# Kernel tuning notes

Hardware: AMD Instinct MI355X
Metric: run time of the kernel (lower is better)

Reference implementation:

```python
import jax, jax.numpy as jnp
import numpy as np

N_NODES = 50000
N_RAND_EDGES = 800000
IN_DIM = 128
HEADS = 4
OUT_FEATS = 32
NEG_SLOPE = 0.2  # DGL GATConv default


def setup_inputs() -> dict:
    key = jax.random.key(0)
    k1, k2, k3, k4, k5, k6 = jax.random.split(key, 6)
    h = jax.random.normal(k1, (N_NODES, IN_DIM), dtype=jnp.float32)
    fc_w = jax.random.normal(k2, (HEADS * OUT_FEATS, IN_DIM), dtype=jnp.float32) * 0.1
    attn_l = jax.random.normal(k3, (HEADS, OUT_FEATS), dtype=jnp.float32) * 0.1
    attn_r = jax.random.normal(k4, (HEADS, OUT_FEATS), dtype=jnp.float32) * 0.1
    src_r = jax.random.randint(k5, (N_RAND_EDGES,), 0, N_NODES, dtype=jnp.int32)
    dst_r = jax.random.randint(k6, (N_RAND_EDGES,), 0, N_NODES, dtype=jnp.int32)
    loops = jnp.arange(N_NODES, dtype=jnp.int32)
    src = jnp.concatenate([src_r, loops])  # self-loops ensure in_degree >= 1
    dst = jnp.concatenate([dst_r, loops])
    return {"h": h, "fc_w": fc_w, "attn_l": attn_l, "attn_r": attn_r,
            "src": src, "dst": dst}


def reference(h, fc_w, attn_l, attn_r, src, dst):
    N = h.shape[0]
    # linear projection, reshape to [N, H, D]
    hf = (h @ fc_w.T).reshape(N, HEADS, OUT_FEATS)
    # per-node attention halves: el = <hf, a_l>, er = <hf, a_r>  -> [N, H]
    el = jnp.einsum('nhd,hd->nh', hf, attn_l)
    er = jnp.einsum('nhd,hd->nh', hf, attn_r)
    # edge scores: u_add_v + leaky_relu  -> [E, H]
    e = jax.nn.leaky_relu(el[src] + er[dst], negative_slope=NEG_SLOPE)
    # segment softmax over incoming edges of each dst node
    m = jax.ops.segment_max(e, dst, num_segments=N)
    ex = jnp.exp(e - m[dst])
    s = jax.ops.segment_sum(ex, dst, num_segments=N)
    a = ex / s[dst]  # [E, H]
    # weighted neighbor aggregation: u_mul_e then segment sum
    msg = hf[src] * a[:, :, None]  # [E, H, D]
    out = jax.ops.segment_sum(msg, dst, num_segments=N)  # [N, H, D]
    return out.reshape(N, HEADS * OUT_FEATS), a[:, :, None]
```

## Files before the change

kernel.cpp:

```cpp
#include <hip/hip_runtime.h>
#include <hip/hip_bf16.h>

#define NEG 0.2f
#define BSTRIDE 8192

typedef float vf4 __attribute__((ext_vector_type(4)));
typedef int   vi4 __attribute__((ext_vector_type(4)));
typedef short bf8 __attribute__((ext_vector_type(8)));
typedef float f32x4 __attribute__((ext_vector_type(4)));

__device__ __forceinline__ float leaky(float x){ return x > 0.f ? x : NEG*x; }
__device__ __forceinline__ float sel4(float4 q, int head){
  float lo = (head & 1) ? q.y : q.x;
  float hi = (head & 1) ? q.w : q.z;
  return (head & 2) ? hi : lo;
}
__device__ __forceinline__ float b2f_lo(unsigned u){ return __uint_as_float(u << 16); }
__device__ __forceinline__ float b2f_hi(unsigned u){ return __uint_as_float(u & 0xffff0000u); }
__device__ __forceinline__ float b2f(unsigned short u){ return __uint_as_float((unsigned)u << 16); }
__device__ __forceinline__ unsigned short f2b(float f){
  __hip_bfloat16 b = __float2bfloat16(f);
  return *(unsigned short*)&b;
}
__device__ __forceinline__ void ntstore_f4(float* p, float a, float b, float c, float d){
  vf4 v; v.x = a; v.y = b; v.z = c; v.w = d;
  __builtin_nontemporal_store(v, (vf4*)p);
}

__global__ __launch_bounds__(256) void k_proj(
    const float* __restrict__ h, const float* __restrict__ fcw,
    const float* __restrict__ attn_l, const float* __restrict__ attn_r,
    unsigned short* __restrict__ hf16, float* __restrict__ el, float* __restrict__ er,
    int* __restrict__ bcur, int N)
{
  __shared__ __align__(16) unsigned short fcs[128*128];
  __shared__ __align__(16) unsigned short hs[4][16*128];

  const int tid = threadIdx.x;
  if (blockIdx.x == 0) bcur[tid] = tid * BSTRIDE;

  for (int i = tid; i < 128*16; i += 256) {
    int f = i >> 4, ch = i & 15;
    const float* p = &fcw[(size_t)f*128 + ch*8];
    float4 w0 = *(const float4*)p;
    float4 w1 = *(const float4*)(p + 4);
    unsigned short* q = &fcs[f*128 + (ch ^ (f & 7))*8];
    q[0]=f2b(w0.x); q[1]=f2b(w0.y); q[2]=f2b(w0.z); q[3]=f2b(w0.w);
    q[4]=f2b(w1.x); q[5]=f2b(w1.y); q[6]=f2b(w1.z); q[7]=f2b(w1.w);
  }
  __syncthreads();

  const int wave = tid >> 6, lane = tid & 63;
  const int r = lane & 15, khi = lane >> 4;

  for (int nt = 0; nt < 2; ++nt) {
    const int nb0 = blockIdx.x*128 + nt*64 + wave*16;
    int gn_a = nb0 + r; if (gn_a >= N) gn_a = N-1;
    const float* hp = &h[(size_t)gn_a*128];

    bf8 afr[4];
    #pragma unroll
    for (int ks = 0; ks < 4; ++ks) {
      const float* p = hp + ks*32 + khi*8;
      float4 w0 = *(const float4*)p;
      float4 w1 = *(const float4*)(p + 4);
      bf8 a;
      a[0]=(short)f2b(w0.x); a[1]=(short)f2b(w0.y); a[2]=(short)f2b(w0.z); a[3]=(short)f2b(w0.w);
      a[4]=(short)f2b(w1.x); a[5]=(short)f2b(w1.y); a[6]=(short)f2b(w1.z); a[7]=(short)f2b(w1.w);
      afr[ks] = a;
    }

    f32x4 acc[8];
    #pragma unroll
    for (int ct = 0; ct < 8; ++ct) { acc[ct][0]=0.f; acc[ct][1]=0.f; acc[ct][2]=0.f; acc[ct][3]=0.f; }

    #pragma unroll
    for (int ct = 0; ct < 8; ++ct) {
      const int f = ct*16 + r;
      #pragma unroll
      for (int ks = 0; ks < 4; ++ks) {
        const int ch = (ks*4 + khi) ^ (f & 7);
        bf8 b = *(const bf8*)&fcs[f*128 + ch*8];
        acc[ct] = __builtin_amdgcn_mfma_f32_16x16x32_bf16(afr[ks], b, acc[ct], 0, 0, 0);
      }
    }

    unsigned short* hw = &hs[wave][0];
    #pragma unroll
    for (int ct = 0; ct < 8; ++ct) {
      const int ftile = ct*16 + r;
      #pragma unroll
      for (int j = 0; j < 4; ++j)
        hw[(khi*4 + j)*128 + ftile] = f2b(acc[ct][j]);
    }

    for (int i = lane; i < 16*16; i += 64) {
      int row = i >> 4, ch = i & 15;
      int gn = nb0 + row;
      if (gn < N)
        *(uint4*)&hf16[(size_t)gn*128 + ch*8] = *(const uint4*)&hw[row*128 + ch*8];
    }

    {
      const int row = lane >> 2, head = lane & 3;
      const int gn = nb0 + row;
      const unsigned short* hr = &hw[row*128 + head*32];
      const float* alp = &attn_l[head*32];
      const float* arp = &attn_r[head*32];
      float e_l = 0.f, e_r = 0.f;
      #pragma unroll
      for (int ff = 0; ff < 32; ++ff) {
        float hv = b2f(hr[ff]);
        e_l += hv * alp[ff];
        e_r += hv * arp[ff];
      }
      if (gn < N) {
        el[(size_t)gn*4 + head] = e_l;
        er[(size_t)gn*4 + head] = e_r;
      }
    }
  }
}

#define TILE 4096
__global__ __launch_bounds__(1024) void k_bin(
    const int* __restrict__ src, const int* __restrict__ dst,
    int* __restrict__ bcur, unsigned int* __restrict__ staging, int E)
{
  __shared__ unsigned int lpack[TILE];
  __shared__ unsigned char lbkt[TILE];
  __shared__ unsigned short sidx[TILE];
  __shared__ int lhist[256], lbase[256], lcur[256], gbase[256];

  const int t = threadIdx.x;
  const int e0 = blockIdx.x * TILE;
  const int cnt = min(TILE, E - e0);

  if (t < 256) lhist[t] = 0;
  __syncthreads();

  for (int i = t; i < cnt; i += 1024) {
    int s = __builtin_nontemporal_load(&src[e0 + i]);
    int d = __builtin_nontemporal_load(&dst[e0 + i]);
    lpack[i] = ((unsigned)(d & 255) << 24) | (unsigned)s;
    int b = d >> 8;
    lbkt[i] = (unsigned char)b;
    atomicAdd(&lhist[b], 1);
  }
  __syncthreads();

  __shared__ int ltmp[256];
  if (t < 256) ltmp[t] = lhist[t];
  __syncthreads();
  for (int off = 1; off < 256; off <<= 1) {
    int x = 0;
    if (t < 256 && t >= off) x = ltmp[t - off];
    __syncthreads();
    if (t < 256) ltmp[t] += x;
    __syncthreads();
  }
  if (t < 256) { lbase[t] = ltmp[t] - lhist[t]; lcur[t] = ltmp[t] - lhist[t]; }
  __syncthreads();

  for (int i = t; i < cnt; i += 1024) {
    int p = atomicAdd(&lcur[lbkt[i]], 1);
    sidx[p] = (unsigned short)i;
  }
  if (t < 256) {
    int c = lhist[t];
    gbase[t] = c ? atomicAdd(&bcur[t], c) : 0;
  }
  __syncthreads();

  for (int p = t; p < cnt; p += 1024) {
    int j = sidx[p];
    int b = lbkt[j];
    staging[gbase[b] + (p - lbase[b])] = lpack[j];
  }
}

__global__ __launch_bounds__(1024) void k_debin(
    const unsigned int* __restrict__ staging, const int* __restrict__ bcur,
    int* __restrict__ esrc, int* __restrict__ offsets, int* __restrict__ degs, int N)
{
  __shared__ int lout[BSTRIDE];
  __shared__ int lhist[256], lexcl[256], lcur[256];

  const int t = threadIdx.x;
  const int b = blockIdx.x;
  const int n0 = b << 8;
  const int nb = min(256, N - n0);
  const int out_start = b * BSTRIDE;
  const int cnt = bcur[b] - out_start;

  if (t < 256) lhist[t] = 0;
  __syncthreads();

  for (int i = t; i < cnt; i += 1024)
    atomicAdd(&lhist[staging[out_start + i] >> 24], 1);
  __syncthreads();

  if (t < 256) lexcl[t] = lhist[t];
  __syncthreads();
  for (int off = 1; off < 256; off <<= 1) {
    int x = 0;
    if (t < 256 && t >= off) x = lexcl[t - off];
    __syncthreads();
    if (t < 256) lexcl[t] += x;
    __syncthreads();
  }
  if (t < 256) {
    int ex = lexcl[t] - lhist[t];
    lexcl[t] = ex;
    lcur[t]  = ex;
  }
  __syncthreads();

  for (int i = t; i < cnt; i += 1024) {
    unsigned int w = staging[out_start + i];
    int p = atomicAdd(&lcur[w >> 24], 1);
    lout[p] = (int)(w & 0x00FFFFFFu);
  }
  __syncthreads();
  for (int i = t; i < cnt; i += 1024)
    esrc[out_start + i] = lout[i];

  if (t < nb) {
    offsets[n0 + t] = out_start + lexcl[t];
    degs[n0 + t]    = lhist[t];
  }
}

__global__ __launch_bounds__(256) void k_aggr(
    const int* __restrict__ esrc, const int* __restrict__ offsets, const int* __restrict__ degs,
    const unsigned short* __restrict__ hf16, const float* __restrict__ el, const float* __restrict__ er,
    float* __restrict__ out, float* __restrict__ mr, int N)
{
  __shared__ float as[4][64][4];
  __shared__ int   es[4][64];
  const int wave = threadIdx.x >> 6, lane = threadIdx.x & 63;
  const int v = blockIdx.x*4 + wave;
  if (v >= N) return;
  const int start = offsets[v];
  const int deg   = degs[v];
  const float4 er4 = *(const float4*)&er[(size_t)v*4];

  const bool act = lane < deg;
  float4 x4 = make_float4(0.f, 0.f, 0.f, 0.f);
  int mys = 0;
  if (act) {
    mys = esrc[start + lane];
    float4 el4 = *(const float4*)&el[(size_t)mys*4];
    x4.x = __expf(leaky(el4.x + er4.x));
    x4.y = __expf(leaky(el4.y + er4.y));
    x4.z = __expf(leaky(el4.z + er4.z));
    x4.w = __expf(leaky(el4.w + er4.w));
  }
  float4 s4 = x4;
  for (int j = lane + 64; j < deg; j += 64) {
    int s = esrc[start + j];
    float4 el4 = *(const float4*)&el[(size_t)s*4];
    s4.x += __expf(leaky(el4.x + er4.x));
    s4.y += __expf(leaky(el4.y + er4.y));
    s4.z += __expf(leaky(el4.z + er4.z));
    s4.w += __expf(leaky(el4.w + er4.w));
  }
  #pragma unroll
  for (int mm = 32; mm; mm >>= 1) {
    s4.x += __shfl_xor(s4.x, mm);
    s4.y += __shfl_xor(s4.y, mm);
    s4.z += __shfl_xor(s4.z, mm);
    s4.w += __shfl_xor(s4.w, mm);
  }
  const float4 r4 = make_float4(1.f/s4.x, 1.f/s4.y, 1.f/s4.z, 1.f/s4.w);

  if (act) {
    float4 a4 = make_float4(x4.x*r4.x, x4.y*r4.y, x4.z*r4.z, x4.w*r4.w);
    *(float4*)&as[wave][lane][0] = a4;
    es[wave][lane] = mys;
  }
  if (lane == 0) *(float4*)&mr[(size_t)v*4] = r4;

  const int g = lane >> 3;
  const int l = lane & 7;
  const int head = l >> 1;
  float acc[16];
  #pragma unroll
  for (int k = 0; k < 16; ++k) acc[k] = 0.f;

  const int degL = deg < 64 ? deg : 64;
  {
    int je = g;
    int jec = je < degL ? je : 0;
    int sj = es[wave][jec];
    float a = je < degL ? as[wave][jec][head] : 0.f;
    const unsigned short* hp = &hf16[(size_t)sj*128 + 16*l];
    uint4 q0 = *(const uint4*)hp;
    uint4 q1 = *(const uint4*)(hp + 8);
    for (int j = 0; j < degL; j += 8) {
      int je2 = j + 8 + g;
      int jec2 = je2 < degL ? je2 : 0;
      int s2 = es[wave][jec2];
      float a2 = je2 < degL ? as[wave][jec2][head] : 0.f;
      const unsigned short* hp2 = &hf16[(size_t)s2*128 + 16*l];
      uint4 p0 = *(const uint4*)hp2;
      uint4 p1 = *(const uint4*)(hp2 + 8);
      acc[0]  += a*b2f_lo(q0.x); acc[1]  += a*b2f_hi(q0.x);
      acc[2]  += a*b2f_lo(q0.y); acc[3]  += a*b2f_hi(q0.y);
      acc[4]  += a*b2f_lo(q0.z); acc[5]  += a*b2f_hi(q0.z);
      acc[6]  += a*b2f_lo(q0.w); acc[7]  += a*b2f_hi(q0.w);
      acc[8]  += a*b2f_lo(q1.x); acc[9]  += a*b2f_hi(q1.x);
      acc[10] += a*b2f_lo(q1.y); acc[11] += a*b2f_hi(q1.y);
      acc[12] += a*b2f_lo(q1.z); acc[13] += a*b2f_hi(q1.z);
      acc[14] += a*b2f_lo(q1.w); acc[15] += a*b2f_hi(q1.w);
      q0 = p0; q1 = p1; a = a2;
    }
  }
  for (int j = 64; j < deg; j += 8) {
    const int je = j + g;
    const bool valid = je < deg;
    int s = esrc[start + (valid ? je : 0)];
    float rh = sel4(r4, head), erh = sel4(er4, head);
    float a = __expf(leaky(el[(size_t)s*4 + head] + erh)) * rh;
    if (!valid) a = 0.f;
    const unsigned short* hp = &hf16[(size_t)s*128 + 16*l];
    uint4 q0 = *(const uint4*)hp;
    uint4 q1 = *(const uint4*)(hp + 8);
    acc[0]  += a*b2f_lo(q0.x); acc[1]  += a*b2f_hi(q0.x);
    acc[2]  += a*b2f_lo(q0.y); acc[3]  += a*b2f_hi(q0.y);
    acc[4]  += a*b2f_lo(q0.z); acc[5]  += a*b2f_hi(q0.z);
    acc[6]  += a*b2f_lo(q0.w); acc[7]  += a*b2f_hi(q0.w);
    acc[8]  += a*b2f_lo(q1.x); acc[9]  += a*b2f_hi(q1.x);
    acc[10] += a*b2f_lo(q1.y); acc[11] += a*b2f_hi(q1.y);
    acc[12] += a*b2f_lo(q1.z); acc[13] += a*b2f_hi(q1.z);
    acc[14] += a*b2f_lo(q1.w); acc[15] += a*b2f_hi(q1.w);
  }

  #pragma unroll
  for (int k = 0; k < 16; ++k) {
    acc[k] += __shfl_xor(acc[k], 8);
    acc[k] += __shfl_xor(acc[k], 16);
    acc[k] += __shfl_xor(acc[k], 32);
  }
  if (g == 0) {
    float* op = &out[(size_t)v*128 + 16*l];
    ntstore_f4(op,      acc[0],  acc[1],  acc[2],  acc[3]);
    ntstore_f4(op + 4,  acc[4],  acc[5],  acc[6],  acc[7]);
    ntstore_f4(op + 8,  acc[8],  acc[9],  acc[10], acc[11]);
    ntstore_f4(op + 12, acc[12], acc[13], acc[14], acc[15]);
  }
}

__global__ void k_attn(const int* __restrict__ src, const int* __restrict__ dst,
                       const float* __restrict__ el, const float* __restrict__ er,
                       const float* __restrict__ mr, float* __restrict__ a_out, int E) {
  int e = blockIdx.x*256 + threadIdx.x;
  if (e >= E) return;
  int s = __builtin_nontemporal_load(&src[e]);
  int d = __builtin_nontemporal_load(&dst[e]);
  float4 el4 = *(const float4*)&el[(size_t)s*4];
  float4 er4 = *(const float4*)&er[(size_t)d*4];
  float4 c4  = *(const float4*)&mr[(size_t)d*4];
  float ax = __expf(leaky(el4.x + er4.x)) * c4.x;
  float ay = __expf(leaky(el4.y + er4.y)) * c4.y;
  float az = __expf(leaky(el4.z + er4.z)) * c4.z;
  float aw = __expf(leaky(el4.w + er4.w)) * c4.w;
  ntstore_f4(&a_out[(size_t)e*4], ax, ay, az, aw);
}

extern "C" void kernel_launch(void* const* d_in, const int* in_sizes, int n_in,
                              void* d_out, int out_size, void* d_ws, size_t ws_size,
                              hipStream_t stream) {
  const float* h      = (const float*)d_in[0];
  const float* fcw    = (const float*)d_in[1];
  const float* attn_l = (const float*)d_in[2];
  const float* attn_r = (const float*)d_in[3];
  const int*   src    = (const int*)d_in[4];
  const int*   dst    = (const int*)d_in[5];
  const int N = in_sizes[0] / 128;
  const int E = in_sizes[4];
  const int B = (N + 255) >> 8;

  float* out   = (float*)d_out;
  float* a_out = out + (size_t)N*128;

  char* w = (char*)d_ws;
  unsigned short* hf16 = (unsigned short*)w; w += (size_t)N*128*sizeof(unsigned short);
  float* el      = (float*)w; w += (size_t)N*4*sizeof(float);
  float* er      = (float*)w; w += (size_t)N*4*sizeof(float);
  float* mr      = (float*)w; w += (size_t)N*4*sizeof(float);
  int*   esrc    = (int*)w;   w += (size_t)256*BSTRIDE*sizeof(int);
  unsigned int* staging = (unsigned int*)w; w += (size_t)256*BSTRIDE*sizeof(unsigned int);
  int*   offsets = (int*)w;   w += (size_t)N*sizeof(int);
  int*   degs    = (int*)w;   w += (size_t)N*sizeof(int);
  int*   bcur    = (int*)w;   w += 256*sizeof(int);

  k_proj<<<(N + 127)/128, 256, 0, stream>>>(h, fcw, attn_l, attn_r, hf16, el, er, bcur, N);

  k_bin<<<(E + TILE - 1)/TILE, 1024, 0, stream>>>(src, dst, bcur, staging, E);
  k_debin<<<B, 1024, 0, stream>>>(staging, bcur, esrc, offsets, degs, N);

  k_aggr<<<(N + 3)/4, 256, 0, stream>>>(esrc, offsets, degs, hf16, el, er, out, mr, N);

  k_attn<<<(E + 255)/256, 256, 0, stream>>>(src, dst, el, er, mr, a_out, E);
}
```

Before: 104.7 us.

## Pre-convert fc weights to bf16 once and process four edges per thread in k_attn

Moves the fp32-to-bf16 conversion of the projection weight into a small separate kernel. k_proj then reads the bf16 weights directly from global memory (L2-cached) instead of staging a swizzled 32KB copy in LDS in every block, and runs 64 nodes per block with more blocks. k_attn now handles four edges per thread with vectorized nontemporal index loads and has a scalar tail path. The aim is to remove per-block weight staging, the barrier and the large LDS footprint in the projection, at the cost of one extra launch and uncoalesced global B-fragment loads.

```diff
diff --git a/kernel.cpp b/kernel.cpp
--- a/kernel.cpp
+++ b/kernel.cpp
@@ -22,102 +22,99 @@
   __hip_bfloat16 b = __float2bfloat16(f);
   return *(unsigned short*)&b;
 }
+__device__ __forceinline__ vi4 ntload_i4(const int* p){
+  return __builtin_nontemporal_load((const vi4*)p);
+}
 __device__ __forceinline__ void ntstore_f4(float* p, float a, float b, float c, float d){
   vf4 v; v.x = a; v.y = b; v.z = c; v.w = d;
   __builtin_nontemporal_store(v, (vf4*)p);
 }
 
-__global__ __launch_bounds__(256) void k_proj(
-    const float* __restrict__ h, const float* __restrict__ fcw,
-    const float* __restrict__ attn_l, const float* __restrict__ attn_r,
-    unsigned short* __restrict__ hf16, float* __restrict__ el, float* __restrict__ er,
-    int* __restrict__ bcur, int N)
-{
-  __shared__ __align__(16) unsigned short fcs[128*128];
-  __shared__ __align__(16) unsigned short hs[4][16*128];
-
+__global__ __launch_bounds__(256) void k_wconv(const float* __restrict__ fcw,
+    unsigned short* __restrict__ fcw16, int* __restrict__ bcur) {
   const int tid = threadIdx.x;
   if (blockIdx.x == 0) bcur[tid] = tid * BSTRIDE;
-
-  for (int i = tid; i < 128*16; i += 256) {
-    int f = i >> 4, ch = i & 15;
-    const float* p = &fcw[(size_t)f*128 + ch*8];
+  const int i = (blockIdx.x*256 + tid) * 8;
+  float4 w0 = *(const float4*)&fcw[i];
+  float4 w1 = *(const float4*)&fcw[i + 4];
+  unsigned short q[8];
+  q[0]=f2b(w0.x); q[1]=f2b(w0.y); q[2]=f2b(w0.z); q[3]=f2b(w0.w);
+  q[4]=f2b(w1.x); q[5]=f2b(w1.y); q[6]=f2b(w1.z); q[7]=f2b(w1.w);
+  *(uint4*)&fcw16[i] = *(const uint4*)q;
+}
+
+__global__ __launch_bounds__(256) void k_proj(
+    const float* __restrict__ h, const unsigned short* __restrict__ fcw16,
+    const float* __restrict__ attn_l, const float* __restrict__ attn_r,
+    unsigned short* __restrict__ hf16, float* __restrict__ el, float* __restrict__ er, int N)
+{
+  __shared__ __align__(16) unsigned short hs[4][16*128];
+
+  const int tid = threadIdx.x;
+  const int wave = tid >> 6, lane = tid & 63;
+  const int r = lane & 15, khi = lane >> 4;
+  const int nb0 = blockIdx.x*64 + wave*16;
+  int gn_a = nb0 + r; if (gn_a >= N) gn_a = N-1;
+  const float* hp = &h[(size_t)gn_a*128];
+
+  bf8 afr[4];
+  #pragma unroll
+  for (int ks = 0; ks < 4; ++ks) {
+    const float* p = hp + ks*32 + khi*8;
     float4 w0 = *(const float4*)p;
     float4 w1 = *(const float4*)(p + 4);
-    unsigned short* q = &fcs[f*128 + (ch ^ (f & 7))*8];
-    q[0]=f2b(w0.x); q[1]=f2b(w0.y); q[2]=f2b(w0.z); q[3]=f2b(w0.w);
-    q[4]=f2b(w1.x); q[5]=f2b(w1.y); q[6]=f2b(w1.z); q[7]=f2b(w1.w);
-  }
-  __syncthreads();
-
-  const int wave = tid >> 6, lane = tid & 63;
-  const int r = lane & 15, khi = lane >> 4;
-
-  for (int nt = 0; nt < 2; ++nt) {
-    const int nb0 = blockIdx.x*128 + nt*64 + wave*16;
-    int gn_a = nb0 + r; if (gn_a >= N) gn_a = N-1;
-    const float* hp = &h[(size_t)gn_a*128];
-
-    bf8 afr[4];
+    bf8 a;
+    a[0]=(short)f2b(w0.x); a[1]=(short)f2b(w0.y); a[2]=(short)f2b(w0.z); a[3]=(short)f2b(w0.w);
+    a[4]=(short)f2b(w1.x); a[5]=(short)f2b(w1.y); a[6]=(short)f2b(w1.z); a[7]=(short)f2b(w1.w);
+    afr[ks] = a;
+  }
+
+  f32x4 acc[8];
+  #pragma unroll
+  for (int ct = 0; ct < 8; ++ct) { acc[ct][0]=0.f; acc[ct][1]=0.f; acc[ct][2]=0.f; acc[ct][3]=0.f; }
+
+  #pragma unroll
+  for (int ct = 0; ct < 8; ++ct) {
+    const int f = ct*16 + r;
     #pragma unroll
     for (int ks = 0; ks < 4; ++ks) {
-      const float* p = hp + ks*32 + khi*8;
-      float4 w0 = *(const float4*)p;
-      float4 w1 = *(const float4*)(p + 4);
-      bf8 a;
-      a[0]=(short)f2b(w0.x); a[1]=(short)f2b(w0.y); a[2]=(short)f2b(w0.z); a[3]=(short)f2b(w0.w);
-      a[4]=(short)f2b(w1.x); a[5]=(short)f2b(w1.y); a[6]=(short)f2b(w1.z); a[7]=(short)f2b(w1.w);
-      afr[ks] = a;
-    }
-
-    f32x4 acc[8];
+      bf8 b = *(const bf8*)&fcw16[(size_t)f*128 + ks*32 + khi*8];
+      acc[ct] = __builtin_amdgcn_mfma_f32_16x16x32_bf16(afr[ks], b, acc[ct], 0, 0, 0);
+    }
+  }
+
+  unsigned short* hw = &hs[wave][0];
+  #pragma unroll
+  for (int ct = 0; ct < 8; ++ct) {
+    const int ftile = ct*16 + r;
     #pragma unroll
-    for (int ct = 0; ct < 8; ++ct) { acc[ct][0]=0.f; acc[ct][1]=0.f; acc[ct][2]=0.f; acc[ct][3]=0.f; }
-
+    for (int j = 0; j < 4; ++j)
+      hw[(khi*4 + j)*128 + ftile] = f2b(acc[ct][j]);
+  }
+
+  for (int i = lane; i < 16*16; i += 64) {
+    int row = i >> 4, ch = i & 15;
+    int gn = nb0 + row;
+    if (gn < N)
+      *(uint4*)&hf16[(size_t)gn*128 + ch*8] = *(const uint4*)&hw[row*128 + ch*8];
+  }
+
+  {
+    const int row = lane >> 2, head = lane & 3;
+    const int gn = nb0 + row;
+    const unsigned short* hr = &hw[row*128 + head*32];
+    const float* alp = &attn_l[head*32];
+    const float* arp = &attn_r[head*32];
+    float e_l = 0.f, e_r = 0.f;
     #pragma unroll
-    for (int ct = 0; ct < 8; ++ct) {
-      const int f = ct*16 + r;
-      #pragma unroll
-      for (int ks = 0; ks < 4; ++ks) {
-        const int ch = (ks*4 + khi) ^ (f & 7);
-        bf8 b = *(const bf8*)&fcs[f*128 + ch*8];
-        acc[ct] = __builtin_amdgcn_mfma_f32_16x16x32_bf16(afr[ks], b, acc[ct], 0, 0, 0);
-      }
-    }
-
-    unsigned short* hw = &hs[wave][0];
-    #pragma unroll
-    for (int ct = 0; ct < 8; ++ct) {
-      const int ftile = ct*16 + r;
-      #pragma unroll
-      for (int j = 0; j < 4; ++j)
-        hw[(khi*4 + j)*128 + ftile] = f2b(acc[ct][j]);
-    }
-
-    for (int i = lane; i < 16*16; i += 64) {
-      int row = i >> 4, ch = i & 15;
-      int gn = nb0 + row;
-      if (gn < N)
-        *(uint4*)&hf16[(size_t)gn*128 + ch*8] = *(const uint4*)&hw[row*128 + ch*8];
-    }
-
-    {
-      const int row = lane >> 2, head = lane & 3;
-      const int gn = nb0 + row;
-      const unsigned short* hr = &hw[row*128 + head*32];
-      const float* alp = &attn_l[head*32];
-      const float* arp = &attn_r[head*32];
-      float e_l = 0.f, e_r = 0.f;
-      #pragma unroll
-      for (int ff = 0; ff < 32; ++ff) {
-        float hv = b2f(hr[ff]);
-        e_l += hv * alp[ff];
-        e_r += hv * arp[ff];
-      }
-      if (gn < N) {
-        el[(size_t)gn*4 + head] = e_l;
-        er[(size_t)gn*4 + head] = e_r;
-      }
+    for (int ff = 0; ff < 32; ++ff) {
+      float hv = b2f(hr[ff]);
+      e_l += hv * alp[ff];
+      e_r += hv * arp[ff];
+    }
+    if (gn < N) {
+      el[(size_t)gn*4 + head] = e_l;
+      er[(size_t)gn*4 + head] = e_r;
     }
   }
 }
@@ -354,18 +351,36 @@
 __global__ void k_attn(const int* __restrict__ src, const int* __restrict__ dst,
                        const float* __restrict__ el, const float* __restrict__ er,
                        const float* __restrict__ mr, float* __restrict__ a_out, int E) {
-  int e = blockIdx.x*256 + threadIdx.x;
-  if (e >= E) return;
-  int s = __builtin_nontemporal_load(&src[e]);
-  int d = __builtin_nontemporal_load(&dst[e]);
-  float4 el4 = *(const float4*)&el[(size_t)s*4];
-  float4 er4 = *(const float4*)&er[(size_t)d*4];
-  float4 c4  = *(const float4*)&mr[(size_t)d*4];
-  float ax = __expf(leaky(el4.x + er4.x)) * c4.x;
-  float ay = __expf(leaky(el4.y + er4.y)) * c4.y;
-  float az = __expf(leaky(el4.z + er4.z)) * c4.z;
-  float aw = __expf(leaky(el4.w + er4.w)) * c4.w;
-  ntstore_f4(&a_out[(size_t)e*4], ax, ay, az, aw);
+  int e0 = (blockIdx.x*256 + threadIdx.x)*4;
+  if (e0 + 3 < E) {
+    vi4 sv = ntload_i4(&src[e0]);
+    vi4 dv = ntload_i4(&dst[e0]);
+    #pragma unroll
+    for (int k = 0; k < 4; ++k) {
+      int s = (k==0)?sv.x:(k==1)?sv.y:(k==2)?sv.z:sv.w;
+      int d = (k==0)?dv.x:(k==1)?dv.y:(k==2)?dv.z:dv.w;
+      float4 el4 = *(const float4*)&el[(size_t)s*4];
+      float4 er4 = *(const float4*)&er[(size_t)d*4];
+      float4 c4  = *(const float4*)&mr[(size_t)d*4];
+      ntstore_f4(&a_out[(size_t)(e0+k)*4],
+                 __expf(leaky(el4.x + er4.x)) * c4.x,
+                 __expf(leaky(el4.y + er4.y)) * c4.y,
+                 __expf(leaky(el4.z + er4.z)) * c4.z,
+                 __expf(leaky(el4.w + er4.w)) * c4.w);
+    }
+  } else {
+    for (int e = e0; e < E; ++e) {
+      int s = src[e], d = dst[e];
+      float4 el4 = *(const float4*)&el[(size_t)s*4];
+      float4 er4 = *(const float4*)&er[(size_t)d*4];
+      float4 c4  = *(const float4*)&mr[(size_t)d*4];
+      ntstore_f4(&a_out[(size_t)e*4],
+                 __expf(leaky(el4.x + er4.x)) * c4.x,
+                 __expf(leaky(el4.y + er4.y)) * c4.y,
+                 __expf(leaky(el4.z + er4.z)) * c4.z,
+                 __expf(leaky(el4.w + er4.w)) * c4.w);
+    }
+  }
 }
 
 extern "C" void kernel_launch(void* const* d_in, const int* in_sizes, int n_in,
@@ -386,6 +401,7 @@
 
   char* w = (char*)d_ws;
   unsigned short* hf16 = (unsigned short*)w; w += (size_t)N*128*sizeof(unsigned short);
+  unsigned short* fcw16 = (unsigned short*)w; w += (size_t)128*128*sizeof(unsigned short);
   float* el      = (float*)w; w += (size_t)N*4*sizeof(float);
   float* er      = (float*)w; w += (size_t)N*4*sizeof(float);
   float* mr      = (float*)w; w += (size_t)N*4*sizeof(float);
@@ -395,12 +411,14 @@
   int*   degs    = (int*)w;   w += (size_t)N*sizeof(int);
   int*   bcur    = (int*)w;   w += 256*sizeof(int);
 
-  k_proj<<<(N + 127)/128, 256, 0, stream>>>(h, fcw, attn_l, attn_r, hf16, el, er, bcur, N);
+  k_wconv<<<8, 256, 0, stream>>>(fcw, fcw16, bcur);
+
+  k_proj<<<(N + 63)/64, 256, 0, stream>>>(h, fcw16, attn_l, attn_r, hf16, el, er, N);
 
   k_bin<<<(E + TILE - 1)/TILE, 1024, 0, stream>>>(src, dst, bcur, staging, E);
   k_debin<<<B, 1024, 0, stream>>>(staging, bcur, esrc, offsets, degs, N);
 
   k_aggr<<<(N + 3)/4, 256, 0, stream>>>(esrc, offsets, degs, hf16, el, er, out, mr, N);
 
-  k_attn<<<(E + 255)/256, 256, 0, stream>>>(src, dst, el, er, mr, a_out, E);
-}
+  k_attn<<<(E/4 + 255)/256 + 1, 256, 0, stream>>>(src, dst, el, er, mr, a_out, E);
+}
```

After: 116.3 us. 1.11x slower.
